# Kernel tuning notes

Hardware: AMD Instinct MI355X
Metric: run time of the kernel (lower is better)

The kernel has to match this reference:

```python
import jax, jax.numpy as jnp
import numpy as np

DT = 0.1
LN_EPS = 1e-5
B, T, D_IN, H, N_APP = 128, 2048, 16, 256, 10


def layer_norm(x, g, b):
    mu = jnp.mean(x, axis=-1, keepdims=True)
    var = jnp.mean(jnp.square(x - mu), axis=-1, keepdims=True)
    return (x - mu) * jax.lax.rsqrt(var + LN_EPS) * g + b


def setup_inputs() -> dict:
    key = jax.random.key(0)
    ks = jax.random.split(key, 4)
    x = jax.random.normal(ks[0], (B, T, D_IN), dtype=jnp.float32)
    W_in = jax.random.normal(ks[1], (H, D_IN), dtype=jnp.float32) * (1.0 / np.sqrt(D_IN))
    b_in = jnp.zeros((H,), dtype=jnp.float32)
    tau_param = jnp.ones((H,), dtype=jnp.float32)
    # xavier_uniform for (H, H)
    limit = np.sqrt(6.0 / (H + H))
    W_rec = jax.random.uniform(ks[2], (H, H), dtype=jnp.float32, minval=-limit, maxval=limit)
    g_intra = jnp.ones((H,), dtype=jnp.float32)
    b_intra = jnp.zeros((H,), dtype=jnp.float32)
    g_norm = jnp.ones((H,), dtype=jnp.float32)
    b_norm = jnp.zeros((H,), dtype=jnp.float32)
    W_head = jax.random.normal(ks[3], (H, N_APP), dtype=jnp.float32) * (1.0 / np.sqrt(H))
    b_head = jnp.zeros((N_APP,), dtype=jnp.float32)
    return dict(x=x, W_in=W_in, b_in=b_in, tau_param=tau_param, W_rec=W_rec,
                g_intra=g_intra, b_intra=b_intra, g_norm=g_norm, b_norm=b_norm,
                W_head=W_head, b_head=b_head)


def reference(x, W_in, b_in, tau_param, W_rec, g_intra, b_intra, g_norm, b_norm, W_head, b_head):
    # x: (B, T, D_IN)
    tau = jax.nn.softplus(tau_param)  # (H,), fixed
    # Precompute input projection for all timesteps: (B, T, H)
    inp_proj = jnp.einsum('bti,hi->bth', x, W_in) + b_in
    xs = jnp.swapaxes(inp_proj, 0, 1)  # (T, B, H) for scan

    def step(h, u_t):
        rec = h @ W_rec                       # (B, H)
        f_t = jnp.tanh(layer_norm(u_t + rec, g_intra, b_intra))
        dh = (-h / tau + f_t) * DT
        h_new = jnp.clip(h + dh, -10.0, 10.0)
        return h_new, None

    h0 = jnp.zeros((x.shape[0], W_rec.shape[0]), dtype=x.dtype)
    h, _ = jax.lax.scan(step, h0, xs)
    h = layer_norm(h, g_norm, b_norm)
    return h @ W_head + b_head  # (B, N_APP)
```

## Files before the change

### kernel.cpp

```cpp
#include <hip/hip_runtime.h>


#define BB     128
#define TT     2048
#define DIN    16
#define HH     256
#define NAPP   10
#define NT     256
#define DT_STEP 0.1f
#define LN_EPS_C 1e-5f
#define LOG2E2  2.8853900817779268f

typedef _Float16 half2_t __attribute__((ext_vector_type(2)));

template<int CTRL>
__device__ __forceinline__ float dpp_mov0(float x) {
    return __builtin_bit_cast(float,
        __builtin_amdgcn_update_dpp(0, __builtin_bit_cast(int, x), CTRL, 0xF, 0xF, true));
}

__device__ __forceinline__ void wave_reduce2(float& s1, float& s2) {
    s1 += dpp_mov0<0x111>(s1); s2 += dpp_mov0<0x111>(s2);
    s1 += dpp_mov0<0x112>(s1); s2 += dpp_mov0<0x112>(s2);
    s1 += dpp_mov0<0x114>(s1); s2 += dpp_mov0<0x114>(s2);
    s1 += dpp_mov0<0x118>(s1); s2 += dpp_mov0<0x118>(s2);
    s1 += dpp_mov0<0x142>(s1); s2 += dpp_mov0<0x142>(s2);
    s1 += dpp_mov0<0x143>(s1); s2 += dpp_mov0<0x143>(s2);
}

__device__ __forceinline__ half2_t as_h2(int v) { return __builtin_bit_cast(half2_t, v); }
__device__ __forceinline__ float rl63(float v) {
    return __builtin_bit_cast(float,
        __builtin_amdgcn_readlane(__builtin_bit_cast(int, v), 63));
}
__device__ __forceinline__ float softplus_f(float v) {
    return (v > 20.f) ? v : log1pf(__expf(v));
}
__device__ __forceinline__ float exp2_fast(float v) {
    float r;
    asm("v_exp_f32 %0, %1" : "=v"(r) : "v"(v));
    return r;
}

__global__ __launch_bounds__(NT, 1)
void liquid_scan_kernel(const float* __restrict__ x,
                        const float* __restrict__ W_in,
                        const float* __restrict__ b_in,
                        const float* __restrict__ tau_param,
                        const float* __restrict__ W_rec,
                        const float* __restrict__ g_intra,
                        const float* __restrict__ b_intra,
                        const float* __restrict__ g_norm,
                        const float* __restrict__ b_norm,
                        const float* __restrict__ W_head,
                        const float* __restrict__ b_head,
                        float* __restrict__ out)
{
    const int tid  = threadIdx.x;
    const int b    = blockIdx.x;
    const int lane = tid & 63;
    const int kq   = tid >> 6;
    const int j0   = lane * 4;

    __shared__ __align__(16) float x_lds[TT * DIN];
    __shared__ __align__(16) float part[2][4][HH];

    {
        const float4* xg = (const float4*)(x + (size_t)b * TT * DIN);
        float4* xl = (float4*)x_lds;
        #pragma unroll 4
        for (int i = tid; i < TT * DIN / 4; i += NT) xl[i] = xg[i];
    }

    half2_t w2[4][32];
    #pragma unroll
    for (int p = 0; p < 32; ++p) {
        const float* r0 = W_rec + (size_t)(64 * kq + 2 * p) * HH + j0;
        const float* r1 = r0 + HH;
        #pragma unroll
        for (int c = 0; c < 4; ++c) {
            half2_t t2; t2.x = (_Float16)r0[c]; t2.y = (_Float16)r1[c];
            w2[c][p] = t2;
        }
    }

    float win[4][4];
    #pragma unroll
    for (int c = 0; c < 4; ++c) {
        #pragma unroll
        for (int r = 0; r < 4; ++r)
            win[c][r] = W_in[(size_t)(j0 + c) * DIN + 4 * kq + r];
    }

    float bi_[4], gi2_[4], bbi2_[4], dec_[4], gn_[4], bn_[4];
    {
        const float4 v0 = *(const float4*)(b_in      + j0);
        const float4 v1 = *(const float4*)(g_intra   + j0);
        const float4 v2 = *(const float4*)(b_intra   + j0);
        const float4 v3 = *(const float4*)(tau_param + j0);
        const float4 v4 = *(const float4*)(g_norm    + j0);
        const float4 v5 = *(const float4*)(b_norm    + j0);
        bi_[0] = v0.x; bi_[1] = v0.y; bi_[2] = v0.z; bi_[3] = v0.w;
        gi2_[0] = v1.x * LOG2E2; gi2_[1] = v1.y * LOG2E2;
        gi2_[2] = v1.z * LOG2E2; gi2_[3] = v1.w * LOG2E2;
        bbi2_[0] = v2.x * LOG2E2; bbi2_[1] = v2.y * LOG2E2;
        bbi2_[2] = v2.z * LOG2E2; bbi2_[3] = v2.w * LOG2E2;
        dec_[0] = 1.f - DT_STEP / softplus_f(v3.x);
        dec_[1] = 1.f - DT_STEP / softplus_f(v3.y);
        dec_[2] = 1.f - DT_STEP / softplus_f(v3.z);
        dec_[3] = 1.f - DT_STEP / softplus_f(v3.w);
        gn_[0] = v4.x; gn_[1] = v4.y; gn_[2] = v4.z; gn_[3] = v4.w;
        bn_[0] = v5.x; bn_[1] = v5.y; bn_[2] = v5.z; bn_[3] = v5.w;
    }

    float hj[4] = {0.f, 0.f, 0.f, 0.f};
    int pkX = 0, pkY = 0;
    const int rlbase = 16 * kq;
    const int o1 = (kq + 1) & 3, o2 = (kq + 2) & 3, o3 = (kq + 3) & 3;

    __syncthreads();

    #pragma unroll 1
    for (int t = 0; t < TT; ++t) {
        const float4 xs = *(const float4*)&x_lds[t * DIN + 4 * kq];

        float acc[4][4];
        #pragma unroll
        for (int c = 0; c < 4; ++c) {
            #pragma unroll
            for (int i = 0; i < 4; ++i) acc[c][i] = 0.f;
        }
        #pragma unroll
        for (int g = 0; g < 8; ++g) {
            const int r0 = __builtin_amdgcn_readlane(pkX, rlbase + 2 * g);
            const int r1 = __builtin_amdgcn_readlane(pkY, rlbase + 2 * g);
            const int r2 = __builtin_amdgcn_readlane(pkX, rlbase + 2 * g + 1);
            const int r3 = __builtin_amdgcn_readlane(pkY, rlbase + 2 * g + 1);
            #pragma unroll
            for (int c = 0; c < 4; ++c)
                acc[c][0] = __builtin_amdgcn_fdot2(as_h2(r0), w2[c][4 * g + 0], acc[c][0], false);
            #pragma unroll
            for (int c = 0; c < 4; ++c)
                acc[c][1] = __builtin_amdgcn_fdot2(as_h2(r1), w2[c][4 * g + 1], acc[c][1], false);
            #pragma unroll
            for (int c = 0; c < 4; ++c)
                acc[c][2] = __builtin_amdgcn_fdot2(as_h2(r2), w2[c][4 * g + 2], acc[c][2], false);
            #pragma unroll
            for (int c = 0; c < 4; ++c)
                acc[c][3] = __builtin_amdgcn_fdot2(as_h2(r3), w2[c][4 * g + 3], acc[c][3], false);
        }
        const float xsv[4] = {xs.x, xs.y, xs.z, xs.w};
        #pragma unroll
        for (int c = 0; c < 4; ++c) {
            #pragma unroll
            for (int i = 0; i < 4; ++i)
                acc[c][i] = fmaf(xsv[i], win[c][i], acc[c][i]);
        }
        float a[4];
        #pragma unroll
        for (int c = 0; c < 4; ++c)
            a[c] = (acc[c][0] + acc[c][1]) + (acc[c][2] + acc[c][3]);

        ((float4*)part[t & 1][kq])[lane] = make_float4(a[0], a[1], a[2], a[3]);
        __syncthreads();

        const float4 p1 = ((const float4*)part[t & 1][o1])[lane];
        const float4 p2 = ((const float4*)part[t & 1][o2])[lane];
        const float4 p3 = ((const float4*)part[t & 1][o3])[lane];
        float u[4];
        u[0] = (a[0] + p1.x) + (p2.x + p3.x) + bi_[0];
        u[1] = (a[1] + p1.y) + (p2.y + p3.y) + bi_[1];
        u[2] = (a[2] + p1.z) + (p2.z + p3.z) + bi_[2];
        u[3] = (a[3] + p1.w) + (p2.w + p3.w) + bi_[3];

        float s1 = (u[0] + u[1]) + (u[2] + u[3]);
        float s2 = (u[0] * u[0] + u[1] * u[1]) + (u[2] * u[2] + u[3] * u[3]);
        wave_reduce2(s1, s2);
        const float S1 = rl63(s1);
        const float S2 = rl63(s2);
        const float mu  = S1 * (1.f / HH);
        const float var = S2 * (1.f / HH) - mu * mu;
        const float rs  = __builtin_amdgcn_rsqf(var + LN_EPS_C);
        #pragma unroll
        for (int c = 0; c < 4; ++c) {
            const float xn2 = fmaf((u[c] - mu) * rs, gi2_[c], bbi2_[c]);
            const float e   = exp2_fast(xn2);
            const float r   = __builtin_amdgcn_rcpf(e + 1.f);
            const float fdt = fmaf(-2.f * DT_STEP, r, DT_STEP);
            const float v   = fmaf(hj[c], dec_[c], fdt);
            hj[c] = __builtin_amdgcn_fmed3f(v, -10.f, 10.f);
        }
        pkX = __builtin_bit_cast(int, __builtin_amdgcn_cvt_pkrtz(hj[0], hj[1]));
        pkY = __builtin_bit_cast(int, __builtin_amdgcn_cvt_pkrtz(hj[2], hj[3]));
    }

    if (kq == 0) {
        float s1 = (hj[0] + hj[1]) + (hj[2] + hj[3]);
        float s2 = (hj[0] * hj[0] + hj[1] * hj[1]) + (hj[2] * hj[2] + hj[3] * hj[3]);
        wave_reduce2(s1, s2);
        const float S1 = rl63(s1);
        const float S2 = rl63(s2);
        const float mu  = S1 * (1.f / HH);
        const float var = S2 * (1.f / HH) - mu * mu;
        const float rs  = rsqrtf(var + LN_EPS_C);
        float4 ho;
        ho.x = (hj[0] - mu) * rs * gn_[0] + bn_[0];
        ho.y = (hj[1] - mu) * rs * gn_[1] + bn_[1];
        ho.z = (hj[2] - mu) * rs * gn_[2] + bn_[2];
        ho.w = (hj[3] - mu) * rs * gn_[3] + bn_[3];
        ((float4*)part[0][0])[lane] = ho;
    }
    __syncthreads();
    if (tid < NAPP) {
        float o = b_head[tid];
        for (int jj = 0; jj < HH; ++jj)
            o = fmaf(part[0][0][jj], W_head[jj * NAPP + tid], o);
        out[(size_t)b * NAPP + tid] = o;
    }
}

extern "C" void kernel_launch(void* const* d_in, const int* in_sizes, int n_in,
                              void* d_out, int out_size, void* d_ws, size_t ws_size,
                              hipStream_t stream) {
    const float* x       = (const float*)d_in[0];
    const float* W_in    = (const float*)d_in[1];
    const float* b_in    = (const float*)d_in[2];
    const float* tau     = (const float*)d_in[3];
    const float* W_rec   = (const float*)d_in[4];
    const float* g_intra = (const float*)d_in[5];
    const float* b_intra = (const float*)d_in[6];
    const float* g_norm  = (const float*)d_in[7];
    const float* b_norm  = (const float*)d_in[8];
    const float* W_head  = (const float*)d_in[9];
    const float* b_head  = (const float*)d_in[10];
    float* out = (float*)d_out;

    hipLaunchKernelGGL(liquid_scan_kernel, dim3(BB), dim3(NT), 0, stream,
                       x, W_in, b_in, tau, W_rec, g_intra, b_intra,
                       g_norm, b_norm, W_head, b_head, out);
}
```

Measured before the change: 1.576 ms.

## Split recurrent K-reduction across eight waves instead of four

Doubles the block to 512 threads so each of eight waves handles 32 rows of W_rec and 2 input features, halving the per-wave dot-product chain per timestep. Partial sums are exchanged through a larger LDS buffer and each wave now reads seven partials instead of three. This shortens the serial matmul part of each step at the cost of more LDS traffic and a wider barrier per timestep.

Result: slower. 2.004 ms (+27.1%).

```diff
diff --git a/kernel.cpp b/kernel.cpp
--- a/kernel.cpp
+++ b/kernel.cpp
@@ -6,7 +6,8 @@
 #define DIN    16
 #define HH     256
 #define NAPP   10
-#define NT     256
+#define NT     512
+#define NW     8
 #define DT_STEP 0.1f
 #define LN_EPS_C 1e-5f
 #define LOG2E2  2.8853900817779268f
@@ -42,7 +43,7 @@
     return r;
 }
 
-__global__ __launch_bounds__(NT, 1)
+__global__ __launch_bounds__(NT, 2)
 void liquid_scan_kernel(const float* __restrict__ x,
                         const float* __restrict__ W_in,
                         const float* __restrict__ b_in,
@@ -59,11 +60,11 @@
     const int tid  = threadIdx.x;
     const int b    = blockIdx.x;
     const int lane = tid & 63;
-    const int kq   = tid >> 6;
+    const int w    = tid >> 6;
     const int j0   = lane * 4;
 
     __shared__ __align__(16) float x_lds[TT * DIN];
-    __shared__ __align__(16) float part[2][4][HH];
+    __shared__ __align__(16) float part[2][NW][HH];
 
     {
         const float4* xg = (const float4*)(x + (size_t)b * TT * DIN);
@@ -72,10 +73,10 @@
         for (int i = tid; i < TT * DIN / 4; i += NT) xl[i] = xg[i];
     }
 
-    half2_t w2[4][32];
+    half2_t w2[4][16];
     #pragma unroll
-    for (int p = 0; p < 32; ++p) {
-        const float* r0 = W_rec + (size_t)(64 * kq + 2 * p) * HH + j0;
+    for (int p = 0; p < 16; ++p) {
+        const float* r0 = W_rec + (size_t)(32 * w + 2 * p) * HH + j0;
         const float* r1 = r0 + HH;
         #pragma unroll
         for (int c = 0; c < 4; ++c) {
@@ -84,12 +85,11 @@
         }
     }
 
-    float win[4][4];
+    float win[4][2];
     #pragma unroll
     for (int c = 0; c < 4; ++c) {
-        #pragma unroll
-        for (int r = 0; r < 4; ++r)
-            win[c][r] = W_in[(size_t)(j0 + c) * DIN + 4 * kq + r];
+        win[c][0] = W_in[(size_t)(j0 + c) * DIN + 2 * w];
+        win[c][1] = W_in[(size_t)(j0 + c) * DIN + 2 * w + 1];
     }
 
     float bi_[4], gi2_[4], bbi2_[4], dec_[4], gn_[4], bn_[4];
@@ -115,14 +115,13 @@
 
     float hj[4] = {0.f, 0.f, 0.f, 0.f};
     int pkX = 0, pkY = 0;
-    const int rlbase = 16 * kq;
-    const int o1 = (kq + 1) & 3, o2 = (kq + 2) & 3, o3 = (kq + 3) & 3;
+    const int rlbase = 8 * w;
 
     __syncthreads();
 
     #pragma unroll 1
     for (int t = 0; t < TT; ++t) {
-        const float4 xs = *(const float4*)&x_lds[t * DIN + 4 * kq];
+        const float2 xs = *(const float2*)&x_lds[t * DIN + 2 * w];
 
         float acc[4][4];
         #pragma unroll
@@ -131,7 +130,7 @@
             for (int i = 0; i < 4; ++i) acc[c][i] = 0.f;
         }
         #pragma unroll
-        for (int g = 0; g < 8; ++g) {
+        for (int g = 0; g < 4; ++g) {
             const int r0 = __builtin_amdgcn_readlane(pkX, rlbase + 2 * g);
             const int r1 = __builtin_amdgcn_readlane(pkY, rlbase + 2 * g);
             const int r2 = __builtin_amdgcn_readlane(pkX, rlbase + 2 * g + 1);
@@ -149,29 +148,25 @@
             for (int c = 0; c < 4; ++c)
                 acc[c][3] = __builtin_amdgcn_fdot2(as_h2(r3), w2[c][4 * g + 3], acc[c][3], false);
         }
-        const float xsv[4] = {xs.x, xs.y, xs.z, xs.w};
-        #pragma unroll
-        for (int c = 0; c < 4; ++c) {
-            #pragma unroll
-            for (int i = 0; i < 4; ++i)
-                acc[c][i] = fmaf(xsv[i], win[c][i], acc[c][i]);
+        #pragma unroll
+        for (int c = 0; c < 4; ++c) {
+            acc[c][0] = fmaf(xs.x, win[c][0], acc[c][0]);
+            acc[c][1] = fmaf(xs.y, win[c][1], acc[c][1]);
         }
         float a[4];
         #pragma unroll
         for (int c = 0; c < 4; ++c)
             a[c] = (acc[c][0] + acc[c][1]) + (acc[c][2] + acc[c][3]);
 
-        ((float4*)part[t & 1][kq])[lane] = make_float4(a[0], a[1], a[2], a[3]);
+        ((float4*)part[t & 1][w])[lane] = make_float4(a[0], a[1], a[2], a[3]);
         __syncthreads();
 
-        const float4 p1 = ((const float4*)part[t & 1][o1])[lane];
-        const float4 p2 = ((const float4*)part[t & 1][o2])[lane];
-        const float4 p3 = ((const float4*)part[t & 1][o3])[lane];
-        float u[4];
-        u[0] = (a[0] + p1.x) + (p2.x + p3.x) + bi_[0];
-        u[1] = (a[1] + p1.y) + (p2.y + p3.y) + bi_[1];
-        u[2] = (a[2] + p1.z) + (p2.z + p3.z) + bi_[2];
-        u[3] = (a[3] + p1.w) + (p2.w + p3.w) + bi_[3];
+        float u[4] = {a[0] + bi_[0], a[1] + bi_[1], a[2] + bi_[2], a[3] + bi_[3]};
+        #pragma unroll
+        for (int i = 1; i < NW; ++i) {
+            const float4 p = ((const float4*)part[t & 1][(w + i) & (NW - 1)])[lane];
+            u[0] += p.x; u[1] += p.y; u[2] += p.z; u[3] += p.w;
+        }
 
         float s1 = (u[0] + u[1]) + (u[2] + u[3]);
         float s2 = (u[0] * u[0] + u[1] * u[1]) + (u[2] * u[2] + u[3] * u[3]);
@@ -194,7 +189,7 @@
         pkY = __builtin_bit_cast(int, __builtin_amdgcn_cvt_pkrtz(hj[2], hj[3]));
     }
 
-    if (kq == 0) {
+    if (w == 0) {
         float s1 = (hj[0] + hj[1]) + (hj[2] + hj[3]);
         float s2 = (hj[0] * hj[0] + hj[1] * hj[1]) + (hj[2] * hj[2] + hj[3] * hj[3]);
         wave_reduce2(s1, s2);
```

## Process two batch rows per block and store inputs as fp16 in LDS

Applied to the files above, without the earlier changes.

Each 512-thread block now runs the recurrence for two batch elements, one per group of four waves, so the grid halves to 64 blocks and each SIMD interleaves two independent serial chains. To make room for two input sequences in LDS, x is converted to packed fp16 on load. The input projection then uses fdot2 with fp16-packed W_in instead of fp32 FMAs. This trades more latency hiding per SIMD for a shared block-wide barrier across 8 waves, reduced input precision, and a tighter register budget from launch_bounds(512,2) that may cause spills given the 128 registers of cached W_rec.

Measured after the change: 2.685 ms. +70.3%, slower.

```diff
diff --git a/kernel.cpp b/kernel.cpp
--- a/kernel.cpp
+++ b/kernel.cpp
@@ -6,12 +6,17 @@
 #define DIN    16
 #define HH     256
 #define NAPP   10
-#define NT     256
+#define NT     512
+#define NG     2
 #define DT_STEP 0.1f
 #define LN_EPS_C 1e-5f
 #define LOG2E2  2.8853900817779268f
 
 typedef _Float16 half2_t __attribute__((ext_vector_type(2)));
+
+__device__ __forceinline__ unsigned pkrtz_u32(float a, float b) {
+    return __builtin_bit_cast(unsigned, __builtin_amdgcn_cvt_pkrtz(a, b));
+}
 
 template<int CTRL>
 __device__ __forceinline__ float dpp_mov0(float x) {
@@ -42,7 +47,7 @@
     return r;
 }
 
-__global__ __launch_bounds__(NT, 1)
+__global__ __launch_bounds__(NT, 2)
 void liquid_scan_kernel(const float* __restrict__ x,
                         const float* __restrict__ W_in,
                         const float* __restrict__ b_in,
@@ -57,19 +62,25 @@
                         float* __restrict__ out)
 {
     const int tid  = threadIdx.x;
-    const int b    = blockIdx.x;
+    const int g    = tid >> 8;
+    const int t4   = tid & 255;
     const int lane = tid & 63;
-    const int kq   = tid >> 6;
+    const int kq   = (tid >> 6) & 3;
     const int j0   = lane * 4;
-
-    __shared__ __align__(16) float x_lds[TT * DIN];
-    __shared__ __align__(16) float part[2][4][HH];
+    const int batch = blockIdx.x * NG + g;
+
+    __shared__ __align__(16) unsigned x16[NG][TT * DIN / 2];
+    __shared__ __align__(16) float    part[2][NG][4][HH];
 
     {
-        const float4* xg = (const float4*)(x + (size_t)b * TT * DIN);
-        float4* xl = (float4*)x_lds;
-        #pragma unroll 4
-        for (int i = tid; i < TT * DIN / 4; i += NT) xl[i] = xg[i];
+        const int total = NG * (TT * DIN / 2);
+        for (int i = tid; i < total; i += NT) {
+            const int gg  = i >> 14;
+            const int off = i & 16383;
+            const float2 v =
+                ((const float2*)(x + (size_t)(blockIdx.x * NG + gg) * TT * DIN))[off];
+            x16[gg][off] = pkrtz_u32(v.x, v.y);
+        }
     }
 
     half2_t w2[4][32];
@@ -84,12 +95,12 @@
         }
     }
 
-    float win[4][4];
+    half2_t win2[4][2];
     #pragma unroll
     for (int c = 0; c < 4; ++c) {
-        #pragma unroll
-        for (int r = 0; r < 4; ++r)
-            win[c][r] = W_in[(size_t)(j0 + c) * DIN + 4 * kq + r];
+        const float* wr = W_in + (size_t)(j0 + c) * DIN + 4 * kq;
+        win2[c][0] = as_h2((int)pkrtz_u32(wr[0], wr[1]));
+        win2[c][1] = as_h2((int)pkrtz_u32(wr[2], wr[3]));
     }
 
     float bi_[4], gi2_[4], bbi2_[4], dec_[4], gn_[4], bn_[4];
@@ -122,7 +133,7 @@
 
     #pragma unroll 1
     for (int t = 0; t < TT; ++t) {
-        const float4 xs = *(const float4*)&x_lds[t * DIN + 4 * kq];
+        const uint2 xsp = *(const uint2*)&x16[g][t * (DIN / 2) + 2 * kq];
 
         float acc[4][4];
         #pragma unroll
@@ -131,42 +142,40 @@
             for (int i = 0; i < 4; ++i) acc[c][i] = 0.f;
         }
         #pragma unroll
-        for (int g = 0; g < 8; ++g) {
-            const int r0 = __builtin_amdgcn_readlane(pkX, rlbase + 2 * g);
-            const int r1 = __builtin_amdgcn_readlane(pkY, rlbase + 2 * g);
-            const int r2 = __builtin_amdgcn_readlane(pkX, rlbase + 2 * g + 1);
-            const int r3 = __builtin_amdgcn_readlane(pkY, rlbase + 2 * g + 1);
-            #pragma unroll
-            for (int c = 0; c < 4; ++c)
-                acc[c][0] = __builtin_amdgcn_fdot2(as_h2(r0), w2[c][4 * g + 0], acc[c][0], false);
-            #pragma unroll
-            for (int c = 0; c < 4; ++c)
-                acc[c][1] = __builtin_amdgcn_fdot2(as_h2(r1), w2[c][4 * g + 1], acc[c][1], false);
-            #pragma unroll
-            for (int c = 0; c < 4; ++c)
-                acc[c][2] = __builtin_amdgcn_fdot2(as_h2(r2), w2[c][4 * g + 2], acc[c][2], false);
-            #pragma unroll
-            for (int c = 0; c < 4; ++c)
-                acc[c][3] = __builtin_amdgcn_fdot2(as_h2(r3), w2[c][4 * g + 3], acc[c][3], false);
-        }
-        const float xsv[4] = {xs.x, xs.y, xs.z, xs.w};
-        #pragma unroll
-        for (int c = 0; c < 4; ++c) {
-            #pragma unroll
-            for (int i = 0; i < 4; ++i)
-                acc[c][i] = fmaf(xsv[i], win[c][i], acc[c][i]);
+        for (int gg = 0; gg < 8; ++gg) {
+            const int r0 = __builtin_amdgcn_readlane(pkX, rlbase + 2 * gg);
+            const int r1 = __builtin_amdgcn_readlane(pkY, rlbase + 2 * gg);
+            const int r2 = __builtin_amdgcn_readlane(pkX, rlbase + 2 * gg + 1);
+            const int r3 = __builtin_amdgcn_readlane(pkY, rlbase + 2 * gg + 1);
+            #pragma unroll
+            for (int c = 0; c < 4; ++c)
+                acc[c][0] = __builtin_amdgcn_fdot2(as_h2(r0), w2[c][4 * gg + 0], acc[c][0], false);
+            #pragma unroll
+            for (int c = 0; c < 4; ++c)
+                acc[c][1] = __builtin_amdgcn_fdot2(as_h2(r1), w2[c][4 * gg + 1], acc[c][1], false);
+            #pragma unroll
+            for (int c = 0; c < 4; ++c)
+                acc[c][2] = __builtin_amdgcn_fdot2(as_h2(r2), w2[c][4 * gg + 2], acc[c][2], false);
+            #pragma unroll
+            for (int c = 0; c < 4; ++c)
+                acc[c][3] = __builtin_amdgcn_fdot2(as_h2(r3), w2[c][4 * gg + 3], acc[c][3], false);
+        }
+        #pragma unroll
+        for (int c = 0; c < 4; ++c) {
+            acc[c][0] = __builtin_amdgcn_fdot2(as_h2((int)xsp.x), win2[c][0], acc[c][0], false);
+            acc[c][1] = __builtin_amdgcn_fdot2(as_h2((int)xsp.y), win2[c][1], acc[c][1], false);
         }
         float a[4];
         #pragma unroll
         for (int c = 0; c < 4; ++c)
             a[c] = (acc[c][0] + acc[c][1]) + (acc[c][2] + acc[c][3]);
 
-        ((float4*)part[t & 1][kq])[lane] = make_float4(a[0], a[1], a[2], a[3]);
+        ((float4*)part[t & 1][g][kq])[lane] = make_float4(a[0], a[1], a[2], a[3]);
         __syncthreads();
 
-        const float4 p1 = ((const float4*)part[t & 1][o1])[lane];
-        const float4 p2 = ((const float4*)part[t & 1][o2])[lane];
-        const float4 p3 = ((const float4*)part[t & 1][o3])[lane];
+        const float4 p1 = ((const float4*)part[t & 1][g][o1])[lane];
+        const float4 p2 = ((const float4*)part[t & 1][g][o2])[lane];
+        const float4 p3 = ((const float4*)part[t & 1][g][o3])[lane];
         float u[4];
         u[0] = (a[0] + p1.x) + (p2.x + p3.x) + bi_[0];
         u[1] = (a[1] + p1.y) + (p2.y + p3.y) + bi_[1];
@@ -190,8 +199,8 @@
             const float v   = fmaf(hj[c], dec_[c], fdt);
             hj[c] = __builtin_amdgcn_fmed3f(v, -10.f, 10.f);
         }
-        pkX = __builtin_bit_cast(int, __builtin_amdgcn_cvt_pkrtz(hj[0], hj[1]));
-        pkY = __builtin_bit_cast(int, __builtin_amdgcn_cvt_pkrtz(hj[2], hj[3]));
+        pkX = (int)pkrtz_u32(hj[0], hj[1]);
+        pkY = (int)pkrtz_u32(hj[2], hj[3]);
     }
 
     if (kq == 0) {
@@ -208,14 +217,14 @@
         ho.y = (hj[1] - mu) * rs * gn_[1] + bn_[1];
         ho.z = (hj[2] - mu) * rs * gn_[2] + bn_[2];
         ho.w = (hj[3] - mu) * rs * gn_[3] + bn_[3];
-        ((float4*)part[0][0])[lane] = ho;
+        ((float4*)part[0][g][0])[lane] = ho;
     }
     __syncthreads();
-    if (tid < NAPP) {
-        float o = b_head[tid];
+    if (t4 < NAPP) {
+        float o = b_head[t4];
         for (int jj = 0; jj < HH; ++jj)
-            o = fmaf(part[0][0][jj], W_head[jj * NAPP + tid], o);
-        out[(size_t)b * NAPP + tid] = o;
+            o = fmaf(part[0][g][0][jj], W_head[jj * NAPP + t4], o);
+        out[(size_t)batch * NAPP + t4] = o;
     }
 }
 
@@ -235,7 +244,7 @@
     const float* b_head  = (const float*)d_in[10];
     float* out = (float*)d_out;
 
-    hipLaunchKernelGGL(liquid_scan_kernel, dim3(BB), dim3(NT), 0, stream,
+    hipLaunchKernelGGL(liquid_scan_kernel, dim3(BB / NG), dim3(NT), 0, stream,
                        x, W_in, b_in, tau, W_rec, g_intra, b_intra,
                        g_norm, b_norm, W_head, b_head, out);
 }
```
